# Performance work log

Measured on AMD Instinct MI355X. Metric: run time of the kernel, lower is better.

## Reference

```python
import jax, jax.numpy as jnp
import numpy as np

OUT, IN = 11008, 4096  # LLaMA-7B FFN up-projection


def _unpack(packed, shape):
    """Unpack 2-bit fields (4 ternary values per byte, stored as q+1 in {0,1,2})."""
    shifts = jnp.arange(4, dtype=packed.dtype) * 2
    vals = (packed[:, None] >> shifts) & 3            # [n_bytes, 4]
    n = shape[0] * shape[1]
    q = vals.reshape(-1)[:n].astype(jnp.float32) - 1.0  # back to {-1,0,1}
    return q.reshape(shape)


def _pack(q):
    """Pack ternary int values {-1,0,1} -> 2-bit fields, 4 per byte."""
    flat = (q + 1).reshape(-1)
    pad = (-flat.shape[0]) % 4
    flat = jnp.pad(flat, (0, pad))
    groups = flat.reshape(-1, 4)
    weights = (jnp.int32(1) << (jnp.arange(4, dtype=jnp.int32) * 2))
    return jnp.sum(groups * weights, axis=1).astype(jnp.int32)


def setup_inputs() -> dict:
    key = jax.random.key(0)
    kx, kw = jax.random.split(key)
    x = jax.random.normal(kx, (4, 2048, IN), dtype=jnp.float32)
    # build a realistic weight, then absmean-quantize it (per output row)
    W = jax.random.normal(kw, (OUT, IN), dtype=jnp.float32) * 0.02
    weight_scale = jnp.mean(jnp.abs(W), axis=1, keepdims=True)  # [OUT, 1]
    q = jnp.clip(jnp.round(W / weight_scale), -1.0, 1.0).astype(jnp.int32)
    packed_weight = _pack(q)  # [OUT*IN/4] int32 bytes
    return {"x": x, "packed_weight": packed_weight, "weight_scale": weight_scale}


def reference(x, packed_weight, weight_scale):
    # unpack ternary weights, dequantize via per-row scale, dense GEMM
    W = _unpack(packed_weight, (OUT, IN)) * weight_scale  # [OUT, IN] fp32
    return jnp.einsum('bsi,oi->bso', x, W)
```

## Files before the change

kernel.cpp:

```cpp
#include <hip/hip_runtime.h>
#include <hip/hip_bf16.h>


#define M_DIM 8192
#define N_DIM 11008
#define K_DIM 4096
#define BM 128
#define BN 256
#define BK 64
#define KT 64
#define NB_N (N_DIM / BN)
#define NWG ((M_DIM / BM) * NB_N)

#define XBF_BYTES ((size_t)M_DIM * K_DIM * 2)
#define BT_BYTES  ((size_t)N_DIM * K_DIM / 4)
#define WS_NEED   (XBF_BYTES + BT_BYTES)

typedef __attribute__((ext_vector_type(8))) short bf16x8;
typedef __attribute__((ext_vector_type(4))) float f32x4;

__device__ inline unsigned int bf16b(float f) {
  union { __hip_bfloat16 h; unsigned short u; } cv;
  cv.h = __float2bfloat16(f);
  return (unsigned int)cv.u;
}

__device__ __forceinline__ void gload_lds16(const void* g, void* l) {
  __builtin_amdgcn_global_load_lds(
      (const __attribute__((address_space(1))) unsigned int*)g,
      (__attribute__((address_space(3))) unsigned int*)l, 16, 0, 0);
}

#define XCVT_BLOCKS 16384
#define PACK_BLOCKS 5504
__global__ __launch_bounds__(256)
void prep_kernel(const float* __restrict__ X, const int* __restrict__ PW,
                 unsigned short* __restrict__ Xbf, unsigned char* __restrict__ Bt) {
  const int b = blockIdx.x;
  if (b < XCVT_BLOCKS) {
    const size_t i8 = ((size_t)b * 256 + threadIdx.x) * 8;
    float4 a = *(const float4*)(X + i8);
    float4 c = *(const float4*)(X + i8 + 4);
    uint4 o;
    o.x = bf16b(a.x) | (bf16b(a.y) << 16);
    o.y = bf16b(a.z) | (bf16b(a.w) << 16);
    o.z = bf16b(c.x) | (bf16b(c.y) << 16);
    o.w = bf16b(c.z) | (bf16b(c.w) << 16);
    *(uint4*)(Xbf + i8) = o;
  } else {
    const size_t i8 = ((size_t)(b - XCVT_BLOCKS) * 256 + threadIdx.x) * 8;
    int4 p = *(const int4*)(PW + i8);
    int4 q = *(const int4*)(PW + i8 + 4);
    uint2 o;
    o.x = (unsigned)(p.x & 255) | ((unsigned)(p.y & 255) << 8) |
          ((unsigned)(p.z & 255) << 16) | ((unsigned)(p.w & 255) << 24);
    o.y = (unsigned)(q.x & 255) | ((unsigned)(q.y & 255) << 8) |
          ((unsigned)(q.z & 255) << 16) | ((unsigned)(q.w & 255) << 24);
    *(uint2*)(Bt + i8) = o;
  }
}

__global__ __launch_bounds__(256, 2)
void qlin_main_kernel(const unsigned short* __restrict__ Xbf,
                      const unsigned char* __restrict__ Bt,
                      const float* __restrict__ SC, float* __restrict__ OUT) {
  __shared__ unsigned short As[3][BM * BK];
  __shared__ unsigned char  Bs[3][BN * 16];

  const int tid = threadIdx.x;
  const int lane = tid & 63;
  const int w = tid >> 6;

  const int wg = blockIdx.x;
  const int swz = (wg & 7) * (NWG / 8) + (wg >> 3);
  const int bm = swz / NB_N;
  const int bn = swz - bm * NB_N;

  const int l3 = lane >> 3;
  const int asrc_c = (lane & 7) ^ l3;
  const char* ab0 = (const char*)Xbf +
      (size_t)(bm * BM + w * 32 + l3) * (K_DIM * 2) + asrc_c * 16;
  const char* bb = (const char*)Bt + (size_t)(bn * BN + w * 64 + lane) * (K_DIM / 4);

#define STAGE(IDX, KT_) do {                                           \
    unsigned short* ad_ = &As[IDX][w * 2048];                          \
    unsigned char* bd_ = &Bs[IDX][w * 1024];                           \
    gload_lds16(ab0 + (KT_)*128,           ad_);                       \
    gload_lds16(ab0 + (KT_)*128 + 65536,   ad_ + 512);                 \
    gload_lds16(ab0 + (KT_)*128 + 131072,  ad_ + 1024);                \
    gload_lds16(ab0 + (KT_)*128 + 196608,  ad_ + 1536);                \
    gload_lds16(bb  + (KT_)*16,            bd_);                       \
  } while (0)

  f32x4 acc[8][4];
#pragma unroll
  for (int i = 0; i < 8; ++i)
#pragma unroll
    for (int j = 0; j < 4; ++j) acc[i][j] = (f32x4){0.f, 0.f, 0.f, 0.f};

  const int l4 = lane >> 4;
  const int axor = lane & 7;
  const int arow = (lane & 15) * 128;
  const int hb = l4 >> 1;
  const unsigned hoff = (unsigned)(l4 & 1) * 16;
  const int rbase = (w * 64 + (lane & 15)) * 16 + hb * 4;

#define COMPUTE(B_) do {                                                        \
    const char* asb_ = (const char*)&As[B_][0];                                 \
    const unsigned char* bsb_ = &Bs[B_][0];                                     \
    _Pragma("unroll")                                                           \
    for (int kk = 0; kk < 2; ++kk) {                                            \
      bf16x8 af[8];                                                             \
      _Pragma("unroll")                                                         \
      for (int m = 0; m < 8; ++m)                                               \
        af[m] = *(const bf16x8*)(asb_ + m * 2048 + arow +                       \
                                 (((kk * 4 + l4) ^ axor) << 4));                \
      _Pragma("unroll")                                                         \
      for (int n = 0; n < 4; ++n) {                                             \
        const unsigned d = *(const unsigned*)(bsb_ + rbase + n * 256 + kk * 8); \
        const unsigned w16 = (d >> hoff) & 0xFFFFu;                             \
        const unsigned u = w16 | (w16 << 14);                                   \
        union { uint4 s; bf16x8 v; } bfr;                                       \
        bfr.s.x = ((u << 14) & 0xC000C000u) + 0x40004000u;                      \
        bfr.s.y = ((u << 10) & 0xC000C000u) + 0x40004000u;                      \
        bfr.s.z = ((u << 6)  & 0xC000C000u) + 0x40004000u;                      \
        bfr.s.w = ((u << 2)  & 0xC000C000u) + 0x40004000u;                      \
        _Pragma("unroll")                                                       \
        for (int m = 0; m < 8; ++m)                                             \
          acc[m][n] = __builtin_amdgcn_mfma_f32_16x16x32_bf16(af[m], bfr.v,     \
                                                              acc[m][n], 0, 0, 0); \
      }                                                                         \
    }                                                                           \
  } while (0)

  STAGE(0, 0);
  int cur = 0;
  for (int kt = 0; kt < KT - 1; ++kt) {
    const int nxt = (cur == 2) ? 0 : cur + 1;
    STAGE(nxt, kt + 1);
    asm volatile("s_waitcnt vmcnt(5)" ::: "memory");
    asm volatile("s_waitcnt lgkmcnt(0)" ::: "memory");
    __builtin_amdgcn_s_barrier();
    COMPUTE(cur);
    cur = nxt;
  }
  asm volatile("s_waitcnt vmcnt(0)" ::: "memory");
  asm volatile("s_waitcnt lgkmcnt(0)" ::: "memory");
  __builtin_amdgcn_s_barrier();
  COMPUTE(cur);
#undef STAGE
#undef COMPUTE

  const int gc0 = bn * BN + w * 64 + (lane & 15);
  const int gr0 = bm * BM + (l4 << 2);
  float sc[4];
#pragma unroll
  for (int n = 0; n < 4; ++n) sc[n] = -0.5f * SC[gc0 + n * 16];
#pragma unroll
  for (int m = 0; m < 8; ++m)
#pragma unroll
    for (int n = 0; n < 4; ++n)
#pragma unroll
      for (int r = 0; r < 4; ++r)
        OUT[(size_t)(gr0 + m * 16 + r) * N_DIM + gc0 + n * 16] = acc[m][n][r] * sc[n];
}

#define BSTRIDE 20
__global__ __launch_bounds__(256, 2)
void qlin_fused_kernel(const float* __restrict__ X, const int* __restrict__ PW,
                       const float* __restrict__ SC, float* __restrict__ OUT) {
  __shared__ unsigned short Asf[BM * BK];
  __shared__ unsigned char Bp[BN * BSTRIDE];

  const int tid = threadIdx.x;
  const int wg = blockIdx.x;
  const int swz = (wg & 7) * (NWG / 8) + (wg >> 3);
  const int bm = swz / NB_N;
  const int bn = swz - bm * NB_N;

  const int lane = tid & 63;
  const int wave = tid >> 6;
  const int wr = wave >> 1;
  const int wc = wave & 1;

  const int arow = tid >> 3;
  const int ac8  = tid & 7;
  const float* xptr = X + (size_t)(bm * BM + arow) * K_DIM + ac8 * 8;
  const unsigned int aswz = ((unsigned)arow & 7u) << 4;

  const int bc  = tid & 3;
  const int br0 = tid >> 2;
  const int* pwptr = PW + (size_t)(bn * BN + br0) * (K_DIM / 4) + bc * 4;
  const int bwoff = (bc & 1) * 8 + (bc >> 1) * 2;

  f32x4 acc[4][8];
#pragma unroll
  for (int i = 0; i < 4; ++i)
#pragma unroll
    for (int j = 0; j < 8; ++j) acc[i][j] = (f32x4){0.f, 0.f, 0.f, 0.f};

  float4 av[4][2];
  int4 bv[4];
#pragma unroll
  for (int j = 0; j < 4; ++j) {
    av[j][0] = *(const float4*)(xptr + (size_t)(32 * j) * K_DIM);
    av[j][1] = *(const float4*)(xptr + (size_t)(32 * j) * K_DIM + 4);
  }
#pragma unroll
  for (int j = 0; j < 4; ++j)
    bv[j] = *(const int4*)(pwptr + (size_t)(64 * j) * (K_DIM / 4));

  for (int kt = 0; kt < KT; ++kt) {
    __syncthreads();
#pragma unroll
    for (int j = 0; j < 4; ++j) {
      uint4 wv;
      wv.x = bf16b(av[j][0].x) | (bf16b(av[j][0].y) << 16);
      wv.y = bf16b(av[j][0].z) | (bf16b(av[j][0].w) << 16);
      wv.z = bf16b(av[j][1].x) | (bf16b(av[j][1].y) << 16);
      wv.w = bf16b(av[j][1].z) | (bf16b(av[j][1].w) << 16);
      *(uint4*)((char*)Asf + (arow + 32 * j) * 128 + (((unsigned)ac8 * 16u) ^ aswz)) = wv;
    }
#pragma unroll
    for (int j = 0; j < 4; ++j) {
      const unsigned int ulo = ((unsigned)bv[j].x & 255u) | (((unsigned)bv[j].y & 255u) << 8);
      const unsigned int uhi = ((unsigned)bv[j].z & 255u) | (((unsigned)bv[j].w & 255u) << 8);
      unsigned char* dst = Bp + (br0 + 64 * j) * BSTRIDE + bwoff;
      *(unsigned short*)(dst)     = (unsigned short)ulo;
      *(unsigned short*)(dst + 4) = (unsigned short)uhi;
    }
    __syncthreads();

    if (kt + 1 < KT) {
#pragma unroll
      for (int j = 0; j < 4; ++j) {
        av[j][0] = *(const float4*)(xptr + (kt + 1) * BK + (size_t)(32 * j) * K_DIM);
        av[j][1] = *(const float4*)(xptr + (kt + 1) * BK + (size_t)(32 * j) * K_DIM + 4);
      }
#pragma unroll
      for (int j = 0; j < 4; ++j)
        bv[j] = *(const int4*)(pwptr + (kt + 1) * 16 + (size_t)(64 * j) * (K_DIM / 4));
    }

    const int bh = lane >> 4;
    const int bcol0 = wc * 128 + (lane & 15);
    unsigned int d[8];
#pragma unroll
    for (int n = 0; n < 8; ++n)
      d[n] = *(const unsigned int*)(Bp + (bcol0 + n * 16) * BSTRIDE + bh * 4);

    const unsigned int rswz = ((unsigned)lane & 7u) << 4;
#pragma unroll
    for (int kk = 0; kk < 2; ++kk) {
      bf16x8 af[4];
      const unsigned int coff = (((unsigned)(kk * 4 + (lane >> 4))) * 16u) ^ rswz;
#pragma unroll
      for (int m = 0; m < 4; ++m)
        af[m] = *(const bf16x8*)((const char*)Asf + (wr * 64 + m * 16 + (lane & 15)) * 128 + coff);
#pragma unroll
      for (int n = 0; n < 8; ++n) {
        const unsigned int w16 = kk ? (d[n] >> 16) : (d[n] & 0xFFFFu);
        const unsigned int u = w16 | (w16 << 14);
        union { uint4 s; bf16x8 v; } bfr;
        bfr.s.x = ((u << 14) & 0xC000C000u) + 0x40004000u;
        bfr.s.y = ((u << 10) & 0xC000C000u) + 0x40004000u;
        bfr.s.z = ((u << 6)  & 0xC000C000u) + 0x40004000u;
        bfr.s.w = ((u << 2)  & 0xC000C000u) + 0x40004000u;
#pragma unroll
        for (int m = 0; m < 4; ++m)
          acc[m][n] = __builtin_amdgcn_mfma_f32_16x16x32_bf16(af[m], bfr.v, acc[m][n], 0, 0, 0);
      }
    }
  }

  const int gc0 = bn * BN + wc * 128 + (lane & 15);
  const int gr0 = bm * BM + wr * 64 + ((lane >> 4) << 2);
  float sc[8];
#pragma unroll
  for (int n = 0; n < 8; ++n) sc[n] = -0.5f * SC[gc0 + n * 16];
#pragma unroll
  for (int m = 0; m < 4; ++m)
#pragma unroll
    for (int n = 0; n < 8; ++n)
#pragma unroll
      for (int r = 0; r < 4; ++r)
        OUT[(size_t)(gr0 + m * 16 + r) * N_DIM + gc0 + n * 16] = acc[m][n][r] * sc[n];
}

extern "C" void kernel_launch(void* const* d_in, const int* in_sizes, int n_in,
                              void* d_out, int out_size, void* d_ws, size_t ws_size,
                              hipStream_t stream) {
  const float* x  = (const float*)d_in[0];
  const int*   pw = (const int*)d_in[1];
  const float* sc = (const float*)d_in[2];
  float* out = (float*)d_out;
  (void)in_sizes; (void)n_in; (void)out_size;

  if (ws_size >= WS_NEED) {
    unsigned short* xbf = (unsigned short*)d_ws;
    unsigned char* bt = (unsigned char*)d_ws + XBF_BYTES;
    prep_kernel<<<dim3(XCVT_BLOCKS + PACK_BLOCKS), dim3(256), 0, stream>>>(x, pw, xbf, bt);
    qlin_main_kernel<<<dim3(NWG), dim3(256), 0, stream>>>(xbf, bt, sc, out);
  } else {
    qlin_fused_kernel<<<dim3(NWG), dim3(256), 0, stream>>>(x, pw, sc, out);
  }
}
```

Measured before the change: 637.6 us.

## Restructure main GEMM loop into ping-pong phased schedule with setprio and deeper prefetch

The main loop now prefetches two K-tiles ahead and splits each tile's compute into four phases. Each phase interleaves LDS reads for half the A rows with 16 MFMAs and sets wave priority around the MFMA block, with barriers between phases. The goal is to overlap LDS reads and global loads with matrix work and to keep waves from different workgroups alternating. The prep kernel is also split into two separate launches, which adds a launch, and the many extra barriers per tile add synchronisation cost.

Measured after the change: 700.1 us. +9.8%, slower.

```diff
diff --git a/kernel.cpp b/kernel.cpp
--- a/kernel.cpp
+++ b/kernel.cpp
@@ -9,8 +9,8 @@
 #define BN 256
 #define BK 64
 #define KT 64
-#define NB_N (N_DIM / BN)
-#define NWG ((M_DIM / BM) * NB_N)
+#define NB_N 43
+#define NWG 2752
 
 #define XBF_BYTES ((size_t)M_DIM * K_DIM * 2)
 #define BT_BYTES  ((size_t)N_DIM * K_DIM / 4)
@@ -34,36 +34,35 @@
 #define XCVT_BLOCKS 16384
 #define PACK_BLOCKS 5504
 __global__ __launch_bounds__(256)
-void prep_kernel(const float* __restrict__ X, const int* __restrict__ PW,
-                 unsigned short* __restrict__ Xbf, unsigned char* __restrict__ Bt) {
-  const int b = blockIdx.x;
-  if (b < XCVT_BLOCKS) {
-    const size_t i8 = ((size_t)b * 256 + threadIdx.x) * 8;
-    float4 a = *(const float4*)(X + i8);
-    float4 c = *(const float4*)(X + i8 + 4);
-    uint4 o;
-    o.x = bf16b(a.x) | (bf16b(a.y) << 16);
-    o.y = bf16b(a.z) | (bf16b(a.w) << 16);
-    o.z = bf16b(c.x) | (bf16b(c.y) << 16);
-    o.w = bf16b(c.z) | (bf16b(c.w) << 16);
-    *(uint4*)(Xbf + i8) = o;
-  } else {
-    const size_t i8 = ((size_t)(b - XCVT_BLOCKS) * 256 + threadIdx.x) * 8;
-    int4 p = *(const int4*)(PW + i8);
-    int4 q = *(const int4*)(PW + i8 + 4);
-    uint2 o;
-    o.x = (unsigned)(p.x & 255) | ((unsigned)(p.y & 255) << 8) |
-          ((unsigned)(p.z & 255) << 16) | ((unsigned)(p.w & 255) << 24);
-    o.y = (unsigned)(q.x & 255) | ((unsigned)(q.y & 255) << 8) |
-          ((unsigned)(q.z & 255) << 16) | ((unsigned)(q.w & 255) << 24);
-    *(uint2*)(Bt + i8) = o;
-  }
+void xcvt_kernel(const float* __restrict__ X, unsigned short* __restrict__ Xbf) {
+  const size_t i8 = ((size_t)blockIdx.x * 256 + threadIdx.x) * 8;
+  float4 a = *(const float4*)(X + i8);
+  float4 c = *(const float4*)(X + i8 + 4);
+  uint4 o;
+  o.x = bf16b(a.x) | (bf16b(a.y) << 16);
+  o.y = bf16b(a.z) | (bf16b(a.w) << 16);
+  o.z = bf16b(c.x) | (bf16b(c.y) << 16);
+  o.w = bf16b(c.z) | (bf16b(c.w) << 16);
+  *(uint4*)(Xbf + i8) = o;
+}
+
+__global__ __launch_bounds__(256)
+void btight_kernel(const int* __restrict__ PW, unsigned char* __restrict__ Bt) {
+  const size_t i8 = ((size_t)blockIdx.x * 256 + threadIdx.x) * 8;
+  int4 p = *(const int4*)(PW + i8);
+  int4 q = *(const int4*)(PW + i8 + 4);
+  uint2 o;
+  o.x = (unsigned)(p.x & 255) | ((unsigned)(p.y & 255) << 8) |
+        ((unsigned)(p.z & 255) << 16) | ((unsigned)(p.w & 255) << 24);
+  o.y = (unsigned)(q.x & 255) | ((unsigned)(q.y & 255) << 8) |
+        ((unsigned)(q.z & 255) << 16) | ((unsigned)(q.w & 255) << 24);
+  *(uint2*)(Bt + i8) = o;
 }
 
 __global__ __launch_bounds__(256, 2)
-void qlin_main_kernel(const unsigned short* __restrict__ Xbf,
-                      const unsigned char* __restrict__ Bt,
-                      const float* __restrict__ SC, float* __restrict__ OUT) {
+void qlin_p4_kernel(const unsigned short* __restrict__ Xbf,
+                    const unsigned char* __restrict__ Bt,
+                    const float* __restrict__ SC, float* __restrict__ OUT) {
   __shared__ unsigned short As[3][BM * BK];
   __shared__ unsigned char  Bs[3][BN * 16];
 
@@ -77,9 +76,8 @@
   const int bn = swz - bm * NB_N;
 
   const int l3 = lane >> 3;
-  const int asrc_c = (lane & 7) ^ l3;
   const char* ab0 = (const char*)Xbf +
-      (size_t)(bm * BM + w * 32 + l3) * (K_DIM * 2) + asrc_c * 16;
+      (size_t)(bm * BM + w * 32 + l3) * (K_DIM * 2) + ((lane & 7) ^ l3) * 16;
   const char* bb = (const char*)Bt + (size_t)(bn * BN + w * 64 + lane) * (K_DIM / 4);
 
 #define STAGE(IDX, KT_) do {                                           \
@@ -105,51 +103,91 @@
   const unsigned hoff = (unsigned)(l4 & 1) * 16;
   const int rbase = (w * 64 + (lane & 15)) * 16 + hb * 4;
 
-#define COMPUTE(B_) do {                                                        \
-    const char* asb_ = (const char*)&As[B_][0];                                 \
-    const unsigned char* bsb_ = &Bs[B_][0];                                     \
-    _Pragma("unroll")                                                           \
-    for (int kk = 0; kk < 2; ++kk) {                                            \
-      bf16x8 af[8];                                                             \
-      _Pragma("unroll")                                                         \
-      for (int m = 0; m < 8; ++m)                                               \
-        af[m] = *(const bf16x8*)(asb_ + m * 2048 + arow +                       \
-                                 (((kk * 4 + l4) ^ axor) << 4));                \
-      _Pragma("unroll")                                                         \
-      for (int n = 0; n < 4; ++n) {                                             \
-        const unsigned d = *(const unsigned*)(bsb_ + rbase + n * 256 + kk * 8); \
-        const unsigned w16 = (d >> hoff) & 0xFFFFu;                             \
-        const unsigned u = w16 | (w16 << 14);                                   \
-        union { uint4 s; bf16x8 v; } bfr;                                       \
-        bfr.s.x = ((u << 14) & 0xC000C000u) + 0x40004000u;                      \
-        bfr.s.y = ((u << 10) & 0xC000C000u) + 0x40004000u;                      \
-        bfr.s.z = ((u << 6)  & 0xC000C000u) + 0x40004000u;                      \
-        bfr.s.w = ((u << 2)  & 0xC000C000u) + 0x40004000u;                      \
-        _Pragma("unroll")                                                       \
-        for (int m = 0; m < 8; ++m)                                             \
-          acc[m][n] = __builtin_amdgcn_mfma_f32_16x16x32_bf16(af[m], bfr.v,     \
-                                                              acc[m][n], 0, 0, 0); \
-      }                                                                         \
-    }                                                                           \
-  } while (0)
+  bf16x8 af[4];
+  bf16x8 bfr[4];
+  unsigned d4[4];
+
+#define DSA(CB, KK, H) do {                                                    \
+    const char* asb_ = (const char*)&As[CB][0];                                \
+    _Pragma("unroll")                                                          \
+    for (int m = 0; m < 4; ++m)                                                \
+      af[m] = *(const bf16x8*)(asb_ + ((H) * 4 + m) * 2048 + arow +            \
+                               ((((KK) * 4 + l4) ^ axor) << 4));               \
+  } while (0)
+
+#define DSB(CB, KK) do {                                                       \
+    const unsigned char* bsb_ = &Bs[CB][0];                                    \
+    _Pragma("unroll")                                                          \
+    for (int n = 0; n < 4; ++n)                                                \
+      d4[n] = *(const unsigned*)(bsb_ + rbase + n * 256 + (KK) * 8);           \
+  } while (0)
+
+#define UNPACK() do {                                                          \
+    _Pragma("unroll")                                                          \
+    for (int n = 0; n < 4; ++n) {                                              \
+      const unsigned w16 = (d4[n] >> hoff) & 0xFFFFu;                          \
+      const unsigned u = w16 | (w16 << 14);                                    \
+      union { uint4 s; bf16x8 v; } t;                                          \
+      t.s.x = ((u << 14) & 0xC000C000u) + 0x40004000u;                         \
+      t.s.y = ((u << 10) & 0xC000C000u) + 0x40004000u;                         \
+      t.s.z = ((u << 6)  & 0xC000C000u) + 0x40004000u;                         \
+      t.s.w = ((u << 2)  & 0xC000C000u) + 0x40004000u;                         \
+      bfr[n] = t.v;                                                            \
+    }                                                                          \
+  } while (0)
+
+#define MFMA16(H) do {                                                         \
+    _Pragma("unroll")                                                          \
+    for (int m = 0; m < 4; ++m)                                                \
+      _Pragma("unroll")                                                        \
+      for (int n = 0; n < 4; ++n)                                              \
+        acc[(H) * 4 + m][n] = __builtin_amdgcn_mfma_f32_16x16x32_bf16(         \
+            af[m], bfr[n], acc[(H) * 4 + m][n], 0, 0, 0);                      \
+  } while (0)
+
+#define BAR() __builtin_amdgcn_s_barrier()
+#define LGKM0() asm volatile("s_waitcnt lgkmcnt(0)" ::: "memory")
+#define PRIO(P) __builtin_amdgcn_s_setprio(P)
 
   STAGE(0, 0);
-  int cur = 0;
-  for (int kt = 0; kt < KT - 1; ++kt) {
-    const int nxt = (cur == 2) ? 0 : cur + 1;
-    STAGE(nxt, kt + 1);
-    asm volatile("s_waitcnt vmcnt(5)" ::: "memory");
-    asm volatile("s_waitcnt lgkmcnt(0)" ::: "memory");
-    __builtin_amdgcn_s_barrier();
-    COMPUTE(cur);
-    cur = nxt;
+  STAGE(1, 1);
+  asm volatile("s_waitcnt vmcnt(5)" ::: "memory");
+  BAR();
+
+  int cb = 0, sb = 2;
+  for (int kt = 0; kt < KT; ++kt) {
+    const bool more = (kt + 2 < KT);
+    DSA(cb, 0, 0);
+    DSB(cb, 0);
+    if (more) STAGE(sb, kt + 2);
+    BAR(); LGKM0(); PRIO(1);
+    UNPACK();
+    MFMA16(0);
+    PRIO(0); BAR();
+    DSA(cb, 0, 1);
+    BAR(); LGKM0(); PRIO(1);
+    MFMA16(1);
+    PRIO(0); BAR();
+    DSA(cb, 1, 0);
+    DSB(cb, 1);
+    BAR(); LGKM0(); PRIO(1);
+    UNPACK();
+    MFMA16(0);
+    PRIO(0); BAR();
+    DSA(cb, 1, 1);
+    if (more) { asm volatile("s_waitcnt vmcnt(5)" ::: "memory"); }
+    else      { asm volatile("s_waitcnt vmcnt(0)" ::: "memory"); }
+    BAR(); LGKM0(); PRIO(1);
+    MFMA16(1);
+    PRIO(0); BAR();
+    cb = (cb == 2) ? 0 : cb + 1;
+    sb = (sb == 2) ? 0 : sb + 1;
   }
-  asm volatile("s_waitcnt vmcnt(0)" ::: "memory");
-  asm volatile("s_waitcnt lgkmcnt(0)" ::: "memory");
-  __builtin_amdgcn_s_barrier();
-  COMPUTE(cur);
 #undef STAGE
-#undef COMPUTE
+#undef DSA
+#undef DSB
+#undef UNPACK
+#undef MFMA16
 
   const int gc0 = bn * BN + w * 64 + (lane & 15);
   const int gr0 = bm * BM + (l4 << 2);
@@ -169,8 +207,8 @@
 __global__ __launch_bounds__(256, 2)
 void qlin_fused_kernel(const float* __restrict__ X, const int* __restrict__ PW,
                        const float* __restrict__ SC, float* __restrict__ OUT) {
-  __shared__ unsigned short Asf[BM * BK];
-  __shared__ unsigned char Bp[BN * BSTRIDE];
+  __shared__ unsigned short Asf[128 * 64];
+  __shared__ unsigned char Bp[256 * BSTRIDE];
 
   const int tid = threadIdx.x;
   const int wg = blockIdx.x;
@@ -185,12 +223,12 @@
 
   const int arow = tid >> 3;
   const int ac8  = tid & 7;
-  const float* xptr = X + (size_t)(bm * BM + arow) * K_DIM + ac8 * 8;
+  const float* xptr = X + (size_t)(bm * 128 + arow) * K_DIM + ac8 * 8;
   const unsigned int aswz = ((unsigned)arow & 7u) << 4;
 
   const int bc  = tid & 3;
   const int br0 = tid >> 2;
-  const int* pwptr = PW + (size_t)(bn * BN + br0) * (K_DIM / 4) + bc * 4;
+  const int* pwptr = PW + (size_t)(bn * 256 + br0) * (K_DIM / 4) + bc * 4;
   const int bwoff = (bc & 1) * 8 + (bc >> 1) * 2;
 
   f32x4 acc[4][8];
@@ -273,8 +311,8 @@
     }
   }
 
-  const int gc0 = bn * BN + wc * 128 + (lane & 15);
-  const int gr0 = bm * BM + wr * 64 + ((lane >> 4) << 2);
+  const int gc0 = bn * 256 + wc * 128 + (lane & 15);
+  const int gr0 = bm * 128 + wr * 64 + ((lane >> 4) << 2);
   float sc[8];
 #pragma unroll
   for (int n = 0; n < 8; ++n) sc[n] = -0.5f * SC[gc0 + n * 16];
@@ -299,8 +337,9 @@
   if (ws_size >= WS_NEED) {
     unsigned short* xbf = (unsigned short*)d_ws;
     unsigned char* bt = (unsigned char*)d_ws + XBF_BYTES;
-    prep_kernel<<<dim3(XCVT_BLOCKS + PACK_BLOCKS), dim3(256), 0, stream>>>(x, pw, xbf, bt);
-    qlin_main_kernel<<<dim3(NWG), dim3(256), 0, stream>>>(xbf, bt, sc, out);
+    xcvt_kernel<<<dim3(XCVT_BLOCKS), dim3(256), 0, stream>>>(x, xbf);
+    btight_kernel<<<dim3(PACK_BLOCKS), dim3(256), 0, stream>>>(pw, bt);
+    qlin_p4_kernel<<<dim3(NWG), dim3(256), 0, stream>>>(xbf, bt, sc, out);
   } else {
     qlin_fused_kernel<<<dim3(NWG), dim3(256), 0, stream>>>(x, pw, sc, out);
   }
```
